# Kernel tuning notes

Hardware: AMD Instinct MI355X
Metric: run time of the kernel (lower is better)

Reference implementation:

```python
import jax, jax.numpy as jnp
import numpy as np

B, T, E, H = 4, 2048, 1024, 16
HS = E // H  # head_size = 64


def setup_inputs() -> dict:
    key = jax.random.key(0)
    ks = jax.random.split(key, 5)
    x = jax.random.normal(ks[0], (B, T, E), jnp.float32)
    scale = 0.02
    Wq = jax.random.normal(ks[1], (H, E, HS), jnp.float32) * scale
    Wk = jax.random.normal(ks[2], (H, E, HS), jnp.float32) * scale
    Wv = jax.random.normal(ks[3], (H, E, HS), jnp.float32) * scale
    Wo = jax.random.normal(ks[4], (E, E), jnp.float32) * scale
    bo = jnp.zeros((E,), jnp.float32)
    return {"x": x, "Wq": Wq, "Wk": Wk, "Wv": Wv, "Wo": Wo, "bo": bo}


def reference(x, Wq, Wk, Wv, Wo, bo):
    b, t, e = x.shape
    # per-head projections, batched over heads
    Q = jnp.einsum('bte,hed->bhtd', x, Wq)  # (B,H,T,HS)
    K = jnp.einsum('bte,hed->bhtd', x, Wk)
    V = jnp.einsum('bte,hed->bhtd', x, Wv)
    # faithful quirk 1: scale by sqrt(embd_size), not sqrt(head_size)
    scores = jnp.einsum('bhtd,bhsd->bhts', Q, K) / jnp.sqrt(jnp.float32(e))
    mask = jnp.tril(jnp.ones((t, t), dtype=bool))  # (T_q, T_k)
    scores = jnp.where(mask[None, None, :, :], scores, -jnp.inf)
    # faithful quirk 2: original softmaxes over dim=1 of (B,Tq,Tk) = the QUERY axis
    attn = jax.nn.softmax(scores, axis=2)
    out = jnp.einsum('bhts,bhsd->bhtd', attn, V)  # (B,H,T,HS)
    out = out.transpose(0, 2, 1, 3).reshape(b, t, e)  # concat heads -> (B,T,E)
    return out @ Wo + bo
```

## Files before the change

kernel.cpp:

```cpp
#include <hip/hip_runtime.h>
#include <stdint.h>

#define Bn 4
#define Tn 2048
#define En 1024
#define Hn 16
#define HSn 64
#define BHn (Bn*Hn)
#define NRn (Bn*Tn)

#define CEXP 0.0450840831f

typedef __attribute__((ext_vector_type(8))) short short8;
typedef __attribute__((ext_vector_type(4))) float f32x4;
typedef __attribute__((ext_vector_type(16))) float f32x16;
typedef __attribute__((ext_vector_type(4))) unsigned int uint4w;

__device__ __forceinline__ unsigned short f2b(float f){
  union { float f; unsigned int u; } c; c.f = f;
  unsigned int u = c.u + 0x7FFFu + ((c.u >> 16) & 1u);
  return (unsigned short)(u >> 16);
}
__device__ __forceinline__ float b2f(unsigned short s){
  union { unsigned int u; float f; } c; c.u = ((unsigned int)s) << 16;
  return c.f;
}
__device__ __forceinline__ unsigned int cvtpk(float lo, float hi){
  unsigned int r;
  asm("v_cvt_pk_bf16_f32 %0, %1, %2" : "=v"(r) : "v"(lo), "v"(hi));
  return r;
}
__device__ __forceinline__ f32x4 mfma16(short8 a, short8 b, f32x4 c){
  return __builtin_amdgcn_mfma_f32_16x16x32_bf16(a, b, c, 0, 0, 0);
}
__device__ __forceinline__ f32x16 mfma32(short8 a, short8 b, f32x16 c){
  return __builtin_amdgcn_mfma_f32_32x32x16_bf16(a, b, c, 0, 0, 0);
}
__device__ __forceinline__ void gl16(const void* g, void* s){
  __builtin_amdgcn_global_load_lds((const __attribute__((address_space(1))) unsigned int*)g,
                                   (__attribute__((address_space(3))) unsigned int*)s, 16, 0, 0);
}

__global__ void k_cvt_x(const float* __restrict__ x, unsigned short* __restrict__ xb){
  int i = (blockIdx.x * blockDim.x + threadIdx.x) * 8;
  float4 a = *(const float4*)(x + i);
  float4 b = *(const float4*)(x + i + 4);
  alignas(16) unsigned short o[8] = {f2b(a.x),f2b(a.y),f2b(a.z),f2b(a.w),
                                     f2b(b.x),f2b(b.y),f2b(b.z),f2b(b.w)};
  *(uint4w*)(xb + i) = *(const uint4w*)o;
}

__global__ void k_wT(const float* __restrict__ Wq, const float* __restrict__ Wk,
                     const float* __restrict__ Wv, const float* __restrict__ Wo,
                     unsigned short* __restrict__ Wt, unsigned short* __restrict__ Wot)
{
  __shared__ unsigned short Ls[64*80];
  const int tid = threadIdx.x;
  const int ey = blockIdx.x, jt = blockIdx.y;
  const int e0 = ey*64;
  const float* src; int R, c0; unsigned short* outp;
  if (jt < 48){
    int sel = jt >> 4, h = jt & 15;
    const float* W = (sel==0)?Wq:((sel==1)?Wk:Wv);
    src = W + h*(En*HSn); R = HSn; c0 = 0;
    outp = Wt + jt*64*En;
  } else {
    src = Wo; R = En; c0 = (jt-48)*64;
    outp = Wot + (jt-48)*64*En;
  }
  {
    const int e = tid >> 2, cq = (tid & 3)*16;
    const float* p = src + (e0 + e)*R + c0 + cq;
    float vv[16];
    *(float4*)&vv[0]  = *(const float4*)(p);
    *(float4*)&vv[4]  = *(const float4*)(p+4);
    *(float4*)&vv[8]  = *(const float4*)(p+8);
    *(float4*)&vv[12] = *(const float4*)(p+12);
#pragma unroll
    for (int i = 0; i < 16; i++) Ls[(cq+i)*80 + e] = f2b(vv[i]);
  }
  __syncthreads();
  {
    const int c8 = tid & 7, r = tid >> 3;
#pragma unroll
    for (int rr0 = 0; rr0 < 2; rr0++){
      int rr = r + rr0*32;
      *(uint4w*)(outp + rr*En + e0 + c8*8) = *(const uint4w*)&Ls[rr*80 + c8*8];
    }
  }
}

__global__ void __launch_bounds__(256, 2)
k_qkv(const unsigned short* __restrict__ xb,
      const unsigned short* __restrict__ Wt,
      unsigned short* __restrict__ Qb, unsigned short* __restrict__ Kb,
      unsigned short* __restrict__ Vt)
{
  __shared__ unsigned short As[2][128*64];
  __shared__ unsigned short Bs[2][128*64];
  const int tid = threadIdx.x, lane = tid & 63, w = tid >> 6;
  const int wr = w >> 1, wc = w & 1;
  const int mb = blockIdx.x, nb = blockIdx.y;
  const int n0 = nb*128;
  const int sel = n0 >> 10;
  const int nj0 = n0 & 1023;
  const int l15 = lane & 15, kc = lane >> 4;
  const int r8 = lane >> 3, c7 = lane & 7;

  const unsigned short* xbase = xb + (mb*128)*En;
  const unsigned short* wbase = Wt + n0*En;

  f32x4 acc[4][4];
#pragma unroll
  for (int i = 0; i < 4; i++)
#pragma unroll
    for (int j = 0; j < 4; j++) acc[i][j] = (f32x4){0.f,0.f,0.f,0.f};

  auto stage = [&](int buf, int k0){
#pragma unroll
    for (int i = 0; i < 4; i++){
      const int rb = w*32 + i*8;
      const int r = rb + r8;
      const int g = (c7 ^ r8) * 8;
      gl16(xbase + r*En + k0 + g, &As[buf][rb*64]);
      gl16(wbase + r*En + k0 + g, &Bs[buf][rb*64]);
    }
  };

  stage(0, 0);
  __syncthreads();

  for (int kt = 0; kt < 16; kt++){
    const int cur = kt & 1;
    if (kt < 15) stage(cur ^ 1, (kt + 1)*64);
    const unsigned short* Ac = &As[cur][0];
    const unsigned short* Bc = &Bs[cur][0];
#pragma unroll
    for (int ks = 0; ks < 2; ks++){
      short8 af[4], bf[4];
#pragma unroll
      for (int mf = 0; mf < 4; mf++){
        int ar = wr*64 + mf*16 + l15;
        af[mf] = *(const short8*)&Ac[ar*64 + (((ks*4 + kc) ^ (ar & 7))*8)];
      }
#pragma unroll
      for (int nf = 0; nf < 4; nf++){
        int br = wc*64 + nf*16 + l15;
        bf[nf] = *(const short8*)&Bc[br*64 + (((ks*4 + kc) ^ (br & 7))*8)];
      }
#pragma unroll
      for (int mf = 0; mf < 4; mf++)
#pragma unroll
        for (int nf = 0; nf < 4; nf++)
          acc[mf][nf] = mfma16(af[mf], bf[nf], acc[mf][nf]);
    }
    __syncthreads();
  }

  const int q4 = (lane >> 4)*4;
  const int bb = mb >> 4;
  const int tt0 = (mb*128) & 2047;

  if (sel == 2){
    unsigned short* tb = ((w < 2) ? &As[0][0] : &Bs[0][0]) + (w & 1)*8192;
#pragma unroll
    for (int nf = 0; nf < 4; nf++)
#pragma unroll
      for (int mf = 0; mf < 4; mf++){
        uint2 u;
        u.x = cvtpk(acc[mf][nf][0], acc[mf][nf][1]);
        u.y = cvtpk(acc[mf][nf][2], acc[mf][nf][3]);
        *(uint2*)&tb[(nf*16 + l15)*72 + mf*16 + q4] = u;
      }
    const int hh = (nj0 >> 6) + wc;
    unsigned short* vb = Vt + ((bb*Hn + hh)*HSn)*Tn + tt0 + wr*64;
#pragma unroll
    for (int i = 0; i < 8; i++){
      int rr = i*8 + r8;
      *(uint4w*)(vb + rr*Tn + c7*8) = *(const uint4w*)&tb[rr*72 + c7*8];
    }
  } else {
    unsigned short* Out = (sel == 1) ? Kb : Qb;
#pragma unroll
    for (int nf = 0; nf < 4; nf++){
      int jj = nj0 + wc*64 + nf*16 + l15;
      int hh = jj >> 6, dd = jj & 63;
#pragma unroll
      for (int mf = 0; mf < 4; mf++){
#pragma unroll
        for (int q = 0; q < 4; q++){
          int tt = tt0 + wr*64 + mf*16 + q4 + q;
          Out[((bb*Hn + hh)*Tn + tt)*HSn + dd] = f2b(acc[mf][nf][q]);
        }
      }
    }
  }
}

__global__ void k_colsum(const unsigned short* __restrict__ Qb,
                         const unsigned short* __restrict__ Kb,
                         float* __restrict__ Linv)
{
  __shared__ unsigned short Qs[2][128*64];
  __shared__ float Lred[64];
  const int bh = blockIdx.x, ipair = blockIdx.y;
  const int tid = threadIdx.x, lane = tid & 63, w = tid >> 6;
  const int l5 = lane >> 5, l31 = lane & 31;

  for (int ph = 0; ph < 2; ph++){
    const int sb = ph ? (31 - ipair) : ipair;
    const int s0 = sb * 64;

    short8 kf[2][4];
#pragma unroll
    for (int sf = 0; sf < 2; sf++){
      const unsigned short* kr = Kb + (bh*Tn + s0 + sf*32 + l31)*HSn + 8*l5;
#pragma unroll
      for (int ks = 0; ks < 4; ks++) kf[sf][ks] = *(const short8*)(kr + 16*ks);
    }

    float ls[2][16];
#pragma unroll
    for (int sf = 0; sf < 2; sf++)
#pragma unroll
      for (int r = 0; r < 16; r++) ls[sf][r] = 0.f;

    if (tid < 64) Lred[tid] = 0.f;

    const int t0s = (s0 >> 7) << 7;
    const int ntl = (Tn - t0s) >> 7;

    {
      const int c = lane & 7;
#pragma unroll
      for (int i = 0; i < 4; i++){
        int row = (w*4 + i)*8 + (lane >> 3);
        gl16(Qb + (bh*Tn + t0s + row)*HSn + ((c ^ (row & 7))*8), &Qs[0][(w*4 + i)*512]);
      }
    }
    asm volatile("s_waitcnt vmcnt(0)" ::: "memory");
    __syncthreads();

    for (int it = 0; it < ntl; it++){
      const int cur = it & 1;
      if (it + 1 < ntl){
        const int tn = t0s + (it + 1)*128;
        const int c = lane & 7;
#pragma unroll
        for (int i = 0; i < 4; i++){
          int row = (w*4 + i)*8 + (lane >> 3);
          gl16(Qb + (bh*Tn + tn + row)*HSn + ((c ^ (row & 7))*8), &Qs[cur^1][(w*4 + i)*512]);
        }
      }
      const int t0 = t0s + it*128;
      const int tw = t0 + 32*w;
      if (tw + 31 >= s0){
        f32x16 st[2];
#pragma unroll
        for (int sf = 0; sf < 2; sf++)
#pragma unroll
          for (int r = 0; r < 16; r++) st[sf][r] = 0.f;
        const int qrow = w*32 + l31;
        const unsigned short* Qc = &Qs[cur][qrow*64];
        const int sw = qrow & 7;
#pragma unroll
        for (int ks = 0; ks < 4; ks++){
          short8 qb = *(const short8*)&Qc[((l5 + 2*ks) ^ sw)*8];
          st[0] = mfma32(kf[0][ks], qb, st[0]);
          st[1] = mfma32(kf[1][ks], qb, st[1]);
        }
        const int tg = tw + l31;
        if (s0 + 63 <= tw){
#pragma unroll
          for (int sf = 0; sf < 2; sf++)
#pragma unroll
            for (int r = 0; r < 16; r++)
              ls[sf][r] += __builtin_amdgcn_exp2f(st[sf][r] * CEXP);
        } else {
#pragma unroll
          for (int sf = 0; sf < 2; sf++)
#pragma unroll
            for (int r = 0; r < 16; r++){
              int sg = s0 + 32*sf + (r & 3) + 8*(r >> 2) + 4*l5;
              float e = __builtin_amdgcn_exp2f(st[sf][r] * CEXP);
              ls[sf][r] += (tg >= sg) ? e : 0.f;
            }
        }
      }
      asm volatile("s_waitcnt vmcnt(0)" ::: "memory");
      __syncthreads();
    }

#pragma unroll
    for (int sf = 0; sf < 2; sf++)
#pragma unroll
      for (int r = 0; r < 16; r++){
        float v = ls[sf][r];
        v += __shfl_xor(v, 1);  v += __shfl_xor(v, 2);
        v += __shfl_xor(v, 4);  v += __shfl_xor(v, 8);
        v += __shfl_xor(v, 16);
        ls[sf][r] = v;
      }
    if (l31 == 0){
#pragma unroll
      for (int sf = 0; sf < 2; sf++)
#pragma unroll
        for (int r = 0; r < 16; r++){
          int sl = 32*sf + (r & 3) + 8*(r >> 2) + 4*l5;
          atomicAdd(&Lred[sl], ls[sf][r]);
        }
    }
    __syncthreads();
    if (tid < 64) Linv[bh*Tn + s0 + tid] = 1.0f / Lred[tid];
    if (ph == 0) __syncthreads();
  }
}

__global__ void k_vscale(unsigned short* __restrict__ Vt, const float* __restrict__ Linv){
  int i = (blockIdx.x * blockDim.x + threadIdx.x) * 8;
  int bh = i >> 17, t = i & 2047;
  short8 v = *(const short8*)(Vt + i);
  float4 L0 = *(const float4*)(Linv + bh*Tn + t);
  float4 L1 = *(const float4*)(Linv + bh*Tn + t + 4);
  unsigned int r0 = cvtpk(b2f((unsigned short)v[0])*L0.x, b2f((unsigned short)v[1])*L0.y);
  unsigned int r1 = cvtpk(b2f((unsigned short)v[2])*L0.z, b2f((unsigned short)v[3])*L0.w);
  unsigned int r2 = cvtpk(b2f((unsigned short)v[4])*L1.x, b2f((unsigned short)v[5])*L1.y);
  unsigned int r3 = cvtpk(b2f((unsigned short)v[6])*L1.z, b2f((unsigned short)v[7])*L1.w);
  uint4w o; o[0]=r0; o[1]=r1; o[2]=r2; o[3]=r3;
  *(uint4w*)(Vt + i) = o;
}

__global__ void k_attn(const unsigned short* __restrict__ Qb,
                       const unsigned short* __restrict__ Kb,
                       const unsigned short* __restrict__ Vlt,
                       unsigned short* __restrict__ Att)
{
  __shared__ unsigned short Ks[2][64*64];
  __shared__ unsigned short Vs[2][64*64];
  __shared__ unsigned short Ps[4][32*64];
  const int bh = blockIdx.x, ipair = blockIdx.y;
  const int tid = threadIdx.x, lane = tid & 63, w = tid >> 6;
  const int l5 = lane >> 5, l31 = lane & 31;
  const int c7 = lane & 7, r8 = lane >> 3;

  for (int ph = 0; ph < 2; ph++){
    const int tb = ph ? (15 - ipair) : ipair;
    const int t0 = tb * 128;
    const int tbase = t0 + w*32;
    const int nt = (t0 >> 6) + 2;

    short8 qf[4];
    {
      const unsigned short* qr = Qb + (bh*Tn + tbase + l31)*HSn + 8*l5;
#pragma unroll
      for (int ks = 0; ks < 4; ks++) qf[ks] = *(const short8*)(qr + 16*ks);
    }

    f32x16 oacc[2];
#pragma unroll
    for (int df = 0; df < 2; df++)
#pragma unroll
      for (int r = 0; r < 16; r++) oacc[df][r] = 0.f;

    {
#pragma unroll
      for (int i = 0; i < 2; i++){
        int row = (w*2 + i)*8 + r8;
        gl16(Kb  + (bh*Tn + row)*HSn + ((c7 ^ (row & 7))*8), &Ks[0][(w*2 + i)*512]);
        gl16(Vlt + (bh*HSn + row)*Tn + ((c7 ^ (row & 7))*8), &Vs[0][(w*2 + i)*512]);
      }
    }
    asm volatile("s_waitcnt vmcnt(0)" ::: "memory");
    __syncthreads();

    for (int it = 0; it < nt; it++){
      const int cur = it & 1;
      if (it + 1 < nt){
        const int sn = (it + 1)*64;
#pragma unroll
        for (int i = 0; i < 2; i++){
          int row = (w*2 + i)*8 + r8;
          gl16(Kb  + (bh*Tn + sn + row)*HSn + ((c7 ^ (row & 7))*8), &Ks[cur^1][(w*2 + i)*512]);
          gl16(Vlt + (bh*HSn + row)*Tn + sn + ((c7 ^ (row & 7))*8), &Vs[cur^1][(w*2 + i)*512]);
        }
      }
      const int s0 = it * 64;
      if (s0 <= tbase + 31){
        const unsigned short* Kc = &Ks[cur][0];
        const int sw = l31 & 7;
        f32x16 st[2];
#pragma unroll
        for (int sf = 0; sf < 2; sf++)
#pragma unroll
          for (int r = 0; r < 16; r++) st[sf][r] = 0.f;
#pragma unroll
        for (int ks = 0; ks < 4; ks++){
#pragma unroll
          for (int sf = 0; sf < 2; sf++){
            int row = sf*32 + l31;
            short8 ka = *(const short8*)&Kc[row*64 + (((l5 + 2*ks) ^ (row & 7))*8)];
            st[sf] = mfma32(ka, qf[ks], st[sf]);
          }
        }
        unsigned short* Pw = &Ps[w][0];
        const int tg = tbase + l31;
        if (s0 + 63 <= tbase){
#pragma unroll
          for (int sf = 0; sf < 2; sf++)
#pragma unroll
            for (int r2 = 0; r2 < 4; r2++){
              unsigned int a = cvtpk(__builtin_amdgcn_exp2f(st[sf][r2*4+0]*CEXP),
                                     __builtin_amdgcn_exp2f(st[sf][r2*4+1]*CEXP));
              unsigned int b = cvtpk(__builtin_amdgcn_exp2f(st[sf][r2*4+2]*CEXP),
                                     __builtin_amdgcn_exp2f(st[sf][r2*4+3]*CEXP));
              uint2 u; u.x = a; u.y = b;
              *(uint2*)&Pw[l31*64 + (((4*sf + r2) ^ sw)*8) + 4*l5] = u;
            }
        } else {
#pragma unroll
          for (int sf = 0; sf < 2; sf++)
#pragma unroll
            for (int r2 = 0; r2 < 4; r2++){
              int sg = s0 + 32*sf + 8*r2 + 4*l5;
              float p0 = (tg >= sg+0) ? __builtin_amdgcn_exp2f(st[sf][r2*4+0]*CEXP) : 0.f;
              float p1 = (tg >= sg+1) ? __builtin_amdgcn_exp2f(st[sf][r2*4+1]*CEXP) : 0.f;
              float p2 = (tg >= sg+2) ? __builtin_amdgcn_exp2f(st[sf][r2*4+2]*CEXP) : 0.f;
              float p3 = (tg >= sg+3) ? __builtin_amdgcn_exp2f(st[sf][r2*4+3]*CEXP) : 0.f;
              uint2 u; u.x = cvtpk(p0, p1); u.y = cvtpk(p2, p3);
              *(uint2*)&Pw[l31*64 + (((4*sf + r2) ^ sw)*8) + 4*l5] = u;
            }
        }
        const unsigned short* Vc = &Vs[cur][0];
#pragma unroll
        for (int ks = 0; ks < 4; ks++){
          short8 pb = *(const short8*)&Pw[l31*64 + (((2*ks + l5) ^ sw)*8)];
#pragma unroll
          for (int df = 0; df < 2; df++){
            int row = df*32 + l31;
            short8 va = *(const short8*)&Vc[row*64 + (((l5 + 2*ks) ^ (row & 7))*8)];
            oacc[df] = mfma32(va, pb, oacc[df]);
          }
        }
      }
      asm volatile("s_waitcnt vmcnt(0)" ::: "memory");
      __syncthreads();
    }

    {
      const int tg = tbase + l31;
      unsigned short* ob = Att + (bh*Tn + tg)*HSn;
#pragma unroll
      for (int df = 0; df < 2; df++)
#pragma unroll
        for (int r2 = 0; r2 < 4; r2++){
          uint2 u;
          u.x = cvtpk(oacc[df][r2*4+0], oacc[df][r2*4+1]);
          u.y = cvtpk(oacc[df][r2*4+2], oacc[df][r2*4+3]);
          *(uint2*)&ob[32*df + 8*r2 + 4*l5] = u;
        }
    }
  }
}

__global__ void __launch_bounds__(256, 2)
k_oproj(const unsigned short* __restrict__ Att,
        const unsigned short* __restrict__ Wot,
        const float* __restrict__ bo, float* __restrict__ out)
{
  __shared__ unsigned short As[2][128*64];
  __shared__ unsigned short Bs[2][128*64];
  const int tid = threadIdx.x, lane = tid & 63, w = tid >> 6;
  const int wr = w >> 1, wc = w & 1;
  const int mb = blockIdx.x, nb = blockIdx.y;
  const int n0 = nb*128;
  const int l15 = lane & 15, kc = lane >> 4;
  const int r8 = lane >> 3, c7 = lane & 7;
  const int bb = mb >> 4;
  const int t0 = (mb*128) & 2047;

  f32x4 acc[4][4];
#pragma unroll
  for (int i = 0; i < 4; i++)
#pragma unroll
    for (int j = 0; j < 4; j++) acc[i][j] = (f32x4){0.f,0.f,0.f,0.f};

  const unsigned short* wbase = Wot + n0*En;

  auto stage = [&](int buf, int k0){
    const int hh = k0 >> 6;
    const unsigned short* abase = Att + ((bb*Hn + hh)*Tn + t0)*HSn;
#pragma unroll
    for (int i = 0; i < 4; i++){
      const int rb = w*32 + i*8;
      const int r = rb + r8;
      const int g = (c7 ^ r8) * 8;
      gl16(abase + r*HSn + g, &As[buf][rb*64]);
      gl16(wbase + r*En + k0 + g, &Bs[buf][rb*64]);
    }
  };

  stage(0, 0);
  __syncthreads();

  for (int kt = 0; kt < 16; kt++){
    const int cur = kt & 1;
    if (kt < 15) stage(cur ^ 1, (kt + 1)*64);
    const unsigned short* Ac = &As[cur][0];
    const unsigned short* Bc = &Bs[cur][0];
#pragma unroll
    for (int ks = 0; ks < 2; ks++){
      short8 af[4], bf[4];
#pragma unroll
      for (int mf = 0; mf < 4; mf++){
        int ar = wr*64 + mf*16 + l15;
        af[mf] = *(const short8*)&Ac[ar*64 + (((ks*4 + kc) ^ (ar & 7))*8)];
      }
#pragma unroll
      for (int nf = 0; nf < 4; nf++){
        int br = wc*64 + nf*16 + l15;
        bf[nf] = *(const short8*)&Bc[br*64 + (((ks*4 + kc) ^ (br & 7))*8)];
      }
#pragma unroll
      for (int mf = 0; mf < 4; mf++)
#pragma unroll
        for (int nf = 0; nf < 4; nf++)
          acc[mf][nf] = mfma16(af[mf], bf[nf], acc[mf][nf]);
    }
    __syncthreads();
  }

  const int q4 = (lane >> 4)*4;
#pragma unroll
  for (int nf = 0; nf < 4; nf++){
    int j = n0 + wc*64 + nf*16 + l15;
    float bias = bo[j];
#pragma unroll
    for (int mf = 0; mf < 4; mf++){
#pragma unroll
      for (int q = 0; q < 4; q++){
        int rr = mb*128 + wr*64 + mf*16 + q4 + q;
        out[rr*En + j] = acc[mf][nf][q] + bias;
      }
    }
  }
}

extern "C" void kernel_launch(void* const* d_in, const int* in_sizes, int n_in,
                              void* d_out, int out_size, void* d_ws, size_t ws_size,
                              hipStream_t stream)
{
  (void)in_sizes; (void)n_in; (void)out_size; (void)ws_size;
  const float* x  = (const float*)d_in[0];
  const float* Wq = (const float*)d_in[1];
  const float* Wk = (const float*)d_in[2];
  const float* Wv = (const float*)d_in[3];
  const float* Wo = (const float*)d_in[4];
  const float* bo = (const float*)d_in[5];
  float* out = (float*)d_out;

  uint8_t* w = (uint8_t*)d_ws;
  unsigned short* Qb  = (unsigned short*)(w);
  unsigned short* Kb  = (unsigned short*)(w + (16u << 20));
  unsigned short* Vt  = (unsigned short*)(w + (32u << 20));
  unsigned short* xb  = (unsigned short*)(w + (48u << 20));
  unsigned short* Att = (unsigned short*)(w + (48u << 20));
  unsigned short* Wt  = (unsigned short*)(w + (64u << 20));
  unsigned short* Wot = (unsigned short*)(w + (70u << 20));
  float* Linv         = (float*)(w + (72u << 20));

  hipLaunchKernelGGL(k_cvt_x,  dim3(4096),    dim3(256), 0, stream, x, xb);
  hipLaunchKernelGGL(k_wT,     dim3(16, 64),  dim3(256), 0, stream, Wq, Wk, Wv, Wo, Wt, Wot);
  hipLaunchKernelGGL(k_qkv,    dim3(64, 24),  dim3(256), 0, stream, xb, Wt, Qb, Kb, Vt);
  hipLaunchKernelGGL(k_colsum, dim3(64, 16),  dim3(256), 0, stream, Qb, Kb, Linv);
  hipLaunchKernelGGL(k_vscale, dim3(4096),    dim3(256), 0, stream, Vt, Linv);
  hipLaunchKernelGGL(k_attn,   dim3(64, 8),   dim3(256), 0, stream, Qb, Kb, Vt, Att);
  hipLaunchKernelGGL(k_oproj,  dim3(64, 8),   dim3(256), 0, stream, Att, Wot, bo, out);
}
```

Baseline: 226.8 us.

## Keep attention P in registers via permlane swap, split blocks, raise MFMA priority

The attention kernel no longer round-trips the softmax probabilities through shared memory. It packs them to bf16 in registers and uses v_permlane32_swap to form the B operand for the PV MFMA directly. Each block now handles one 128-row query tile, heaviest first, over a grid of twice as many blocks, instead of a balanced pair of tiles. Launch bounds ask for 4 blocks per CU, and s_setprio wraps the MFMA loops in the qkv, colsum, attn and oproj kernels. This trades the paired load balancing for more, smaller blocks and higher occupancy. The permlane layout also has to match the MFMA operand layout exactly.

```diff
diff --git a/kernel.cpp b/kernel.cpp
--- a/kernel.cpp
+++ b/kernel.cpp
@@ -148,11 +148,13 @@
         int br = wc*64 + nf*16 + l15;
         bf[nf] = *(const short8*)&Bc[br*64 + (((ks*4 + kc) ^ (br & 7))*8)];
       }
+      __builtin_amdgcn_s_setprio(1);
 #pragma unroll
       for (int mf = 0; mf < 4; mf++)
 #pragma unroll
         for (int nf = 0; nf < 4; nf++)
           acc[mf][nf] = mfma16(af[mf], bf[nf], acc[mf][nf]);
+      __builtin_amdgcn_s_setprio(0);
     }
     __syncthreads();
   }
@@ -263,12 +265,14 @@
         const int qrow = w*32 + l31;
         const unsigned short* Qc = &Qs[cur][qrow*64];
         const int sw = qrow & 7;
+        __builtin_amdgcn_s_setprio(1);
 #pragma unroll
         for (int ks = 0; ks < 4; ks++){
           short8 qb = *(const short8*)&Qc[((l5 + 2*ks) ^ sw)*8];
           st[0] = mfma32(kf[0][ks], qb, st[0]);
           st[1] = mfma32(kf[1][ks], qb, st[1]);
         }
+        __builtin_amdgcn_s_setprio(0);
         const int tg = tw + l31;
         if (s0 + 63 <= tw){
 #pragma unroll
@@ -330,135 +334,137 @@
   *(uint4w*)(Vt + i) = o;
 }
 
-__global__ void k_attn(const unsigned short* __restrict__ Qb,
-                       const unsigned short* __restrict__ Kb,
-                       const unsigned short* __restrict__ Vlt,
-                       unsigned short* __restrict__ Att)
+__global__ void __launch_bounds__(256, 4)
+k_attn(const unsigned short* __restrict__ Qb,
+       const unsigned short* __restrict__ Kb,
+       const unsigned short* __restrict__ Vlt,
+       unsigned short* __restrict__ Att)
 {
   __shared__ unsigned short Ks[2][64*64];
   __shared__ unsigned short Vs[2][64*64];
-  __shared__ unsigned short Ps[4][32*64];
-  const int bh = blockIdx.x, ipair = blockIdx.y;
+  const int bh = blockIdx.x;
+  const int tb = 15 - blockIdx.y;
+  const int t0 = tb * 128;
   const int tid = threadIdx.x, lane = tid & 63, w = tid >> 6;
   const int l5 = lane >> 5, l31 = lane & 31;
   const int c7 = lane & 7, r8 = lane >> 3;
-
-  for (int ph = 0; ph < 2; ph++){
-    const int tb = ph ? (15 - ipair) : ipair;
-    const int t0 = tb * 128;
-    const int tbase = t0 + w*32;
-    const int nt = (t0 >> 6) + 2;
-
-    short8 qf[4];
-    {
-      const unsigned short* qr = Qb + (bh*Tn + tbase + l31)*HSn + 8*l5;
-#pragma unroll
-      for (int ks = 0; ks < 4; ks++) qf[ks] = *(const short8*)(qr + 16*ks);
-    }
-
-    f32x16 oacc[2];
-#pragma unroll
-    for (int df = 0; df < 2; df++)
-#pragma unroll
-      for (int r = 0; r < 16; r++) oacc[df][r] = 0.f;
-
-    {
+  const int tbase = t0 + w*32;
+  const int nt = 2*tb + 2;
+
+  short8 qf[4];
+  {
+    const unsigned short* qr = Qb + (bh*Tn + tbase + l31)*HSn + 8*l5;
+#pragma unroll
+    for (int ks = 0; ks < 4; ks++) qf[ks] = *(const short8*)(qr + 16*ks);
+  }
+
+  f32x16 oacc[2];
+#pragma unroll
+  for (int df = 0; df < 2; df++)
+#pragma unroll
+    for (int r = 0; r < 16; r++) oacc[df][r] = 0.f;
+
+#pragma unroll
+  for (int i = 0; i < 2; i++){
+    int row = (w*2 + i)*8 + r8;
+    gl16(Kb  + (bh*Tn + row)*HSn + ((c7 ^ (row & 7))*8), &Ks[0][(w*2 + i)*512]);
+    gl16(Vlt + (bh*HSn + row)*Tn + ((c7 ^ (row & 7))*8), &Vs[0][(w*2 + i)*512]);
+  }
+  asm volatile("s_waitcnt vmcnt(0)" ::: "memory");
+  __syncthreads();
+
+  for (int it = 0; it < nt; it++){
+    const int cur = it & 1;
+    if (it + 1 < nt){
+      const int sn = (it + 1)*64;
 #pragma unroll
       for (int i = 0; i < 2; i++){
         int row = (w*2 + i)*8 + r8;
-        gl16(Kb  + (bh*Tn + row)*HSn + ((c7 ^ (row & 7))*8), &Ks[0][(w*2 + i)*512]);
-        gl16(Vlt + (bh*HSn + row)*Tn + ((c7 ^ (row & 7))*8), &Vs[0][(w*2 + i)*512]);
-      }
+        gl16(Kb  + (bh*Tn + sn + row)*HSn + ((c7 ^ (row & 7))*8), &Ks[cur^1][(w*2 + i)*512]);
+        gl16(Vlt + (bh*HSn + row)*Tn + sn + ((c7 ^ (row & 7))*8), &Vs[cur^1][(w*2 + i)*512]);
+      }
+    }
+    const int s0 = it * 64;
+    if (s0 <= tbase + 31){
+      const unsigned short* Kc = &Ks[cur][0];
+      f32x16 st[2];
+#pragma unroll
+      for (int sf = 0; sf < 2; sf++)
+#pragma unroll
+        for (int r = 0; r < 16; r++) st[sf][r] = 0.f;
+      __builtin_amdgcn_s_setprio(1);
+#pragma unroll
+      for (int ks = 0; ks < 4; ks++){
+#pragma unroll
+        for (int sf = 0; sf < 2; sf++){
+          int row = sf*32 + l31;
+          short8 ka = *(const short8*)&Kc[row*64 + (((l5 + 2*ks) ^ (row & 7))*8)];
+          st[sf] = mfma32(ka, qf[ks], st[sf]);
+        }
+      }
+      __builtin_amdgcn_s_setprio(0);
+
+      const int tg = tbase + l31;
+      const bool interior = (s0 + 63 <= tbase);
+#pragma unroll
+      for (int sf = 0; sf < 2; sf++){
+#pragma unroll
+        for (int r = 0; r < 16; r++){
+          float e = __builtin_amdgcn_exp2f(st[sf][r] * CEXP);
+          if (!interior){
+            int sg = s0 + 32*sf + (r & 3) + 8*(r >> 2) + 4*l5;
+            e = (tg >= sg) ? e : 0.f;
+          }
+          st[sf][r] = e;
+        }
+      }
+
+      short8 pb[4];
+#pragma unroll
+      for (int sf = 0; sf < 2; sf++){
+#pragma unroll
+        for (int q = 0; q < 2; q++){
+          unsigned int ax = cvtpk(st[sf][8*q+0], st[sf][8*q+1]);
+          unsigned int ay = cvtpk(st[sf][8*q+2], st[sf][8*q+3]);
+          unsigned int bx = cvtpk(st[sf][8*q+4], st[sf][8*q+5]);
+          unsigned int by = cvtpk(st[sf][8*q+6], st[sf][8*q+7]);
+          asm("v_permlane32_swap_b32 %0, %1" : "+v"(ax), "+v"(bx));
+          asm("v_permlane32_swap_b32 %0, %1" : "+v"(ay), "+v"(by));
+          union { unsigned int u[4]; short8 s; } pk;
+          pk.u[0] = ax; pk.u[1] = ay; pk.u[2] = bx; pk.u[3] = by;
+          pb[sf*2 + q] = pk.s;
+        }
+      }
+
+      const unsigned short* Vc = &Vs[cur][0];
+      __builtin_amdgcn_s_setprio(1);
+#pragma unroll
+      for (int ks = 0; ks < 4; ks++){
+#pragma unroll
+        for (int df = 0; df < 2; df++){
+          int row = df*32 + l31;
+          short8 va = *(const short8*)&Vc[row*64 + (((l5 + 2*ks) ^ (row & 7))*8)];
+          oacc[df] = mfma32(va, pb[ks], oacc[df]);
+        }
+      }
+      __builtin_amdgcn_s_setprio(0);
     }
     asm volatile("s_waitcnt vmcnt(0)" ::: "memory");
     __syncthreads();
-
-    for (int it = 0; it < nt; it++){
-      const int cur = it & 1;
-      if (it + 1 < nt){
-        const int sn = (it + 1)*64;
-#pragma unroll
-        for (int i = 0; i < 2; i++){
-          int row = (w*2 + i)*8 + r8;
-          gl16(Kb  + (bh*Tn + sn + row)*HSn + ((c7 ^ (row & 7))*8), &Ks[cur^1][(w*2 + i)*512]);
-          gl16(Vlt + (bh*HSn + row)*Tn + sn + ((c7 ^ (row & 7))*8), &Vs[cur^1][(w*2 + i)*512]);
-        }
-      }
-      const int s0 = it * 64;
-      if (s0 <= tbase + 31){
-        const unsigned short* Kc = &Ks[cur][0];
-        const int sw = l31 & 7;
-        f32x16 st[2];
-#pragma unroll
-        for (int sf = 0; sf < 2; sf++)
-#pragma unroll
-          for (int r = 0; r < 16; r++) st[sf][r] = 0.f;
-#pragma unroll
-        for (int ks = 0; ks < 4; ks++){
-#pragma unroll
-          for (int sf = 0; sf < 2; sf++){
-            int row = sf*32 + l31;
-            short8 ka = *(const short8*)&Kc[row*64 + (((l5 + 2*ks) ^ (row & 7))*8)];
-            st[sf] = mfma32(ka, qf[ks], st[sf]);
-          }
-        }
-        unsigned short* Pw = &Ps[w][0];
-        const int tg = tbase + l31;
-        if (s0 + 63 <= tbase){
-#pragma unroll
-          for (int sf = 0; sf < 2; sf++)
-#pragma unroll
-            for (int r2 = 0; r2 < 4; r2++){
-              unsigned int a = cvtpk(__builtin_amdgcn_exp2f(st[sf][r2*4+0]*CEXP),
-                                     __builtin_amdgcn_exp2f(st[sf][r2*4+1]*CEXP));
-              unsigned int b = cvtpk(__builtin_amdgcn_exp2f(st[sf][r2*4+2]*CEXP),
-                                     __builtin_amdgcn_exp2f(st[sf][r2*4+3]*CEXP));
-              uint2 u; u.x = a; u.y = b;
-              *(uint2*)&Pw[l31*64 + (((4*sf + r2) ^ sw)*8) + 4*l5] = u;
-            }
-        } else {
-#pragma unroll
-          for (int sf = 0; sf < 2; sf++)
-#pragma unroll
-            for (int r2 = 0; r2 < 4; r2++){
-              int sg = s0 + 32*sf + 8*r2 + 4*l5;
-              float p0 = (tg >= sg+0) ? __builtin_amdgcn_exp2f(st[sf][r2*4+0]*CEXP) : 0.f;
-              float p1 = (tg >= sg+1) ? __builtin_amdgcn_exp2f(st[sf][r2*4+1]*CEXP) : 0.f;
-              float p2 = (tg >= sg+2) ? __builtin_amdgcn_exp2f(st[sf][r2*4+2]*CEXP) : 0.f;
-              float p3 = (tg >= sg+3) ? __builtin_amdgcn_exp2f(st[sf][r2*4+3]*CEXP) : 0.f;
-              uint2 u; u.x = cvtpk(p0, p1); u.y = cvtpk(p2, p3);
-              *(uint2*)&Pw[l31*64 + (((4*sf + r2) ^ sw)*8) + 4*l5] = u;
-            }
-        }
-        const unsigned short* Vc = &Vs[cur][0];
-#pragma unroll
-        for (int ks = 0; ks < 4; ks++){
-          short8 pb = *(const short8*)&Pw[l31*64 + (((2*ks + l5) ^ sw)*8)];
-#pragma unroll
-          for (int df = 0; df < 2; df++){
-            int row = df*32 + l31;
-            short8 va = *(const short8*)&Vc[row*64 + (((l5 + 2*ks) ^ (row & 7))*8)];
-            oacc[df] = mfma32(va, pb, oacc[df]);
-          }
-        }
-      }
-      asm volatile("s_waitcnt vmcnt(0)" ::: "memory");
-      __syncthreads();
-    }
-
-    {
-      const int tg = tbase + l31;
-      unsigned short* ob = Att + (bh*Tn + tg)*HSn;
-#pragma unroll
-      for (int df = 0; df < 2; df++)
-#pragma unroll
-        for (int r2 = 0; r2 < 4; r2++){
-          uint2 u;
-          u.x = cvtpk(oacc[df][r2*4+0], oacc[df][r2*4+1]);
-          u.y = cvtpk(oacc[df][r2*4+2], oacc[df][r2*4+3]);
-          *(uint2*)&ob[32*df + 8*r2 + 4*l5] = u;
-        }
-    }
+  }
+
+  {
+    const int tg = tbase + l31;
+    unsigned short* ob = Att + (bh*Tn + tg)*HSn;
+#pragma unroll
+    for (int df = 0; df < 2; df++)
+#pragma unroll
+      for (int r2 = 0; r2 < 4; r2++){
+        uint2 u;
+        u.x = cvtpk(oacc[df][r2*4+0], oacc[df][r2*4+1]);
+        u.y = cvtpk(oacc[df][r2*4+2], oacc[df][r2*4+3]);
+        *(uint2*)&ob[32*df + 8*r2 + 4*l5] = u;
+      }
   }
 }
 
@@ -520,11 +526,13 @@
         int br = wc*64 + nf*16 + l15;
         bf[nf] = *(const short8*)&Bc[br*64 + (((ks*4 + kc) ^ (br & 7))*8)];
       }
+      __builtin_amdgcn_s_setprio(1);
 #pragma unroll
       for (int mf = 0; mf < 4; mf++)
 #pragma unroll
         for (int nf = 0; nf < 4; nf++)
           acc[mf][nf] = mfma16(af[mf], bf[nf], acc[mf][nf]);
+      __builtin_amdgcn_s_setprio(0);
     }
     __syncthreads();
   }
@@ -573,6 +581,6 @@
   hipLaunchKernelGGL(k_qkv,    dim3(64, 24),  dim3(256), 0, stream, xb, Wt, Qb, Kb, Vt);
   hipLaunchKernelGGL(k_colsum, dim3(64, 16),  dim3(256), 0, stream, Qb, Kb, Linv);
   hipLaunchKernelGGL(k_vscale, dim3(4096),    dim3(256), 0, stream, Vt, Linv);
-  hipLaunchKernelGGL(k_attn,   dim3(64, 8),   dim3(256), 0, stream, Qb, Kb, Vt, Att);
+  hipLaunchKernelGGL(k_attn,   dim3(64, 16),  dim3(256), 0, stream, Qb, Kb, Vt, Att);
   hipLaunchKernelGGL(k_oproj,  dim3(64, 8),   dim3(256), 0, stream, Att, Wot, bo, out);
 }
```

Result: faster. 209.9 us (-7.5%).
